# Kernel optimization log

Measured on AMD Instinct MI355X. Metric: run time of the kernel, lower is better.

The kernel has to match this reference:

```python
import jax, jax.numpy as jnp
import numpy as np


def setup_inputs() -> dict:
    key = jax.random.key(0)
    k1, k2, k3, k4 = jax.random.split(key, 4)
    bs, n, f_in, f_out, n_head = 4, 2048, 64, 64, 8
    h = jax.random.normal(k1, (bs, n, f_in), dtype=jnp.float32)
    adj = jnp.ones((bs, n, n), dtype=bool)  # accepted by forward but unused
    # xavier-uniform-like init scales
    w = jax.random.uniform(k2, (n_head, f_in, f_out), dtype=jnp.float32,
                           minval=-1.0, maxval=1.0) * np.sqrt(6.0 / (f_in + f_out))
    a_src = jax.random.uniform(k3, (n_head, f_out, 1), dtype=jnp.float32,
                               minval=-1.0, maxval=1.0) * np.sqrt(6.0 / (f_out + 1))
    a_dst = jax.random.uniform(k4, (n_head, f_out, 1), dtype=jnp.float32,
                               minval=-1.0, maxval=1.0) * np.sqrt(6.0 / (f_out + 1))
    bias_p = jnp.zeros((f_out,), dtype=jnp.float32)
    return {"h": h, "adj": adj, "w": w, "a_src": a_src, "a_dst": a_dst, "bias_p": bias_p}


def reference(h, adj, w, a_src, a_dst, bias_p):
    # h: [b, n, f_in], w: [h, f_in, f_out]
    h_prime = jnp.einsum('bnf,hfo->bhno', h, w)          # [b, h, n, f_out]
    t = jnp.tanh(h_prime)
    attn_src = jnp.einsum('bhno,ho->bhn', t, a_src[..., 0])  # [b, h, n]
    attn_dst = jnp.einsum('bhno,ho->bhn', t, a_dst[..., 0])  # [b, h, n]
    # attn[b,h,i,j] = src[b,h,i] + dst[b,h,j]  (dense; adj unused in original)
    attn = attn_src[..., :, None] + attn_dst[..., None, :]   # [b, h, n, n]
    attn = jnp.where(attn >= 0, attn, 0.2 * attn)            # leaky_relu(0.2)
    attn = jax.nn.softmax(attn, axis=-1)
    # dropout p=0.0 -> identity
    out = jnp.einsum('bhij,bhjo->bhio', attn, h_prime)       # [b, h, n, f_out]
    return out + bias_p
```

## Files before the change

kernel.cpp:

```cpp
#include <hip/hip_runtime.h>
#include <hip/hip_bf16.h>

#define NN 2048
#define FF 64
#define NH 8
#define BDIM 4
#define BH 32

typedef __attribute__((ext_vector_type(8))) short short8;
typedef __attribute__((ext_vector_type(4))) float floatx4;
typedef __attribute__((ext_vector_type(4))) unsigned uint4v;

__device__ __forceinline__ float LDIN(const void* p, size_t i, int b16) {
    return b16 ? __bfloat162float(((const __hip_bfloat16*)p)[i]) : ((const float*)p)[i];
}
__device__ __forceinline__ unsigned packhi(float f0, float f1) {
    return __builtin_amdgcn_perm(__float_as_uint(f1), __float_as_uint(f0), 0x07060302);
}
__device__ __forceinline__ float hitrunc(float x) {
    return __uint_as_float(__float_as_uint(x) & 0xFFFF0000u);
}
__device__ __forceinline__ ushort bf16bits(float v) {
    __hip_bfloat16 b = __float2bfloat16(v);
    return __builtin_bit_cast(ushort, b);
}
__device__ __forceinline__ int SWZ(int row, int col) {
    return row * 64 + ((((col >> 3) ^ (row & 7)) << 3) | (col & 7));
}
__device__ __forceinline__ float fast_tanh(float v) {
    float ex = __expf(2.0f * v);
    return 1.0f - 2.0f * __builtin_amdgcn_rcpf(ex + 1.0f);
}
__device__ __forceinline__ int sniff_b16(const void* h) {
    unsigned word = ((const unsigned*)h)[threadIdx.x & 63];
    unsigned lowexp = (word >> 7) & 0xFFu;
    bool plaus = (lowexp >= 96u && lowexp <= 159u);
    unsigned long long m = __ballot(plaus);
    return (__popcll(m) >= 48) ? 1 : 0;
}

__global__ __launch_bounds__(256) void k_prep(
    const void* __restrict__ h, const void* __restrict__ w,
    ushort* __restrict__ wF, int* __restrict__ flagOut)
{
    const int hd = blockIdx.x, t = threadIdx.x;
    __shared__ int sb16;
    if (t < 64) {
        int f = sniff_b16(h);
        if (t == 0) { sb16 = f; if (hd == 0) flagOut[0] = f; }
    }
    __syncthreads();
    const int b16 = sb16;

#pragma unroll
    for (int g = 0; g < 2; ++g) {
        int gi = t * 2 + g;
        int ml = gi & 15, q = (gi >> 4) & 3, kc = (gi >> 6) & 1, nt = (gi >> 7) & 3;
        int n = nt * 16 + ml, kb = kc * 32 + q * 8;
        size_t off = (size_t)hd * 4096 + ((nt * 2 + kc) * 4 + q) * 128 + ml * 8;
        if (b16) {
            const ushort* wp = (const ushort*)w + (size_t)hd * FF * FF;
            ushort hi[8];
#pragma unroll
            for (int j = 0; j < 8; ++j) hi[j] = wp[(kb + j) * FF + n];
            *(uint4v*)&wF[off] = __builtin_bit_cast(uint4v, *(short8*)hi);
            short8 z = {0, 0, 0, 0, 0, 0, 0, 0};
            *(uint4v*)&wF[off + 32768] = __builtin_bit_cast(uint4v, z);
        } else {
            const float* wp = (const float*)w + (size_t)hd * FF * FF;
            float x[8];
#pragma unroll
            for (int j = 0; j < 8; ++j) x[j] = wp[(kb + j) * FF + n];
            uint4v hv = { packhi(x[0], x[1]), packhi(x[2], x[3]),
                          packhi(x[4], x[5]), packhi(x[6], x[7]) };
            uint4v lv = { packhi(x[0] - hitrunc(x[0]), x[1] - hitrunc(x[1])),
                          packhi(x[2] - hitrunc(x[2]), x[3] - hitrunc(x[3])),
                          packhi(x[4] - hitrunc(x[4]), x[5] - hitrunc(x[5])),
                          packhi(x[6] - hitrunc(x[6]), x[7] - hitrunc(x[7])) };
            *(uint4v*)&wF[off] = hv;
            *(uint4v*)&wF[off + 32768] = lv;
        }
    }
}

__global__ __launch_bounds__(256) void k_proj(
    const void* __restrict__ h, const ushort* __restrict__ wF,
    const void* __restrict__ asrc, const void* __restrict__ adst,
    ushort* __restrict__ hpTt, float* __restrict__ rArr,
    float* __restrict__ edHa, float* __restrict__ edLa)
{
    const int t  = threadIdx.x;
    const int rt = blockIdx.x & 31;
    const int hd = (blockIdx.x >> 5) & 7;
    const int b  = blockIdx.x >> 8;
    const int bh = b * NH + hd;
    const int r0 = rt * 64;

    __shared__ int sb16;
    __shared__ ushort aHi[64 * 64];
    __shared__ ushort aLo[64 * 64];
    __shared__ ushort trans[64 * 64];
    if (t < 64) {
        int f = sniff_b16(h);
        if (t == 0) sb16 = f;
    }
    __syncthreads();
    const int b16 = sb16;

    const int lane = t & 63, wv = t >> 6;
    const int ml = lane & 15, q = lane >> 4;

    if (b16) {
        const ushort* hsrc = (const ushort*)h + (size_t)(b * NN + r0) * FF;
#pragma unroll
        for (int g0 = 0; g0 < 2; ++g0) {
            int g = t + g0 * 256;
            int row = g >> 3, c8 = (g & 7) * 8;
            uint4v u = *(const uint4v*)(hsrc + row * FF + c8);
            *(uint4v*)&aHi[SWZ(row, c8)] = u;
        }
    } else {
        const float* hsrc = (const float*)h + (size_t)(b * NN + r0) * FF;
#pragma unroll
        for (int g0 = 0; g0 < 4; ++g0) {
            int g = t + g0 * 256;
            int row = g >> 4, c4 = (g & 15) * 4;
            floatx4 x = *(const floatx4*)(hsrc + row * FF + c4);
            uint2 hi2 = { packhi(x[0], x[1]), packhi(x[2], x[3]) };
            uint2 lo2 = { packhi(x[0] - hitrunc(x[0]), x[1] - hitrunc(x[1])),
                          packhi(x[2] - hitrunc(x[2]), x[3] - hitrunc(x[3])) };
            *(uint2*)&aHi[SWZ(row, c4)] = hi2;
            *(uint2*)&aLo[SWZ(row, c4)] = lo2;
        }
    }
    __syncthreads();

    short8 ah[2], al[2];
#pragma unroll
    for (int kc = 0; kc < 2; ++kc) {
        ah[kc] = *(const short8*)&aHi[SWZ(wv * 16 + ml, kc * 32 + q * 8)];
        if (!b16) al[kc] = *(const short8*)&aLo[SWZ(wv * 16 + ml, kc * 32 + q * 8)];
    }
    short8 bhf[4][2], blf[4][2];
    const ushort* wfh = wF + (size_t)hd * 4096;
#pragma unroll
    for (int nt = 0; nt < 4; ++nt)
#pragma unroll
        for (int kc = 0; kc < 2; ++kc) {
            size_t off = ((nt * 2 + kc) * 4 + q) * 128 + ml * 8;
            bhf[nt][kc] = __builtin_bit_cast(short8, *(const uint4v*)&wfh[off]);
            if (!b16) blf[nt][kc] = __builtin_bit_cast(short8, *(const uint4v*)&wfh[off + 32768]);
        }

    float aS[4], aD[4];
#pragma unroll
    for (int nt = 0; nt < 4; ++nt) {
        aS[nt] = LDIN(asrc, hd * FF + nt * 16 + ml, b16);
        aD[nt] = LDIN(adst, hd * FF + nt * 16 + ml, b16);
    }

    floatx4 acc[4];
#pragma unroll
    for (int nt = 0; nt < 4; ++nt) {
        floatx4 a = {0.f, 0.f, 0.f, 0.f};
        if (b16) {
#pragma unroll
            for (int kc = 0; kc < 2; ++kc)
                a = __builtin_amdgcn_mfma_f32_16x16x32_bf16(ah[kc], bhf[nt][kc], a, 0, 0, 0);
        } else {
#pragma unroll
            for (int kc = 0; kc < 2; ++kc) {
                a = __builtin_amdgcn_mfma_f32_16x16x32_bf16(ah[kc], bhf[nt][kc], a, 0, 0, 0);
                a = __builtin_amdgcn_mfma_f32_16x16x32_bf16(ah[kc], blf[nt][kc], a, 0, 0, 0);
                a = __builtin_amdgcn_mfma_f32_16x16x32_bf16(al[kc], bhf[nt][kc], a, 0, 0, 0);
            }
        }
        acc[nt] = a;
    }

#pragma unroll
    for (int nt = 0; nt < 4; ++nt) {
        ushort b0 = bf16bits(acc[nt][0]), b1 = bf16bits(acc[nt][1]);
        ushort b2 = bf16bits(acc[nt][2]), b3 = bf16bits(acc[nt][3]);
        uint2 pk = { (unsigned)b0 | ((unsigned)b1 << 16),
                     (unsigned)b2 | ((unsigned)b3 << 16) };
        *(uint2*)&trans[SWZ(nt * 16 + ml, wv * 16 + q * 4)] = pk;
    }

    float ps[4] = {0.f, 0.f, 0.f, 0.f}, pd[4] = {0.f, 0.f, 0.f, 0.f};
#pragma unroll
    for (int nt = 0; nt < 4; ++nt)
#pragma unroll
        for (int reg = 0; reg < 4; ++reg) {
            float tv = fast_tanh(acc[nt][reg]);
            ps[reg] += tv * aS[nt];
            pd[reg] += tv * aD[nt];
        }
#pragma unroll
    for (int msk = 1; msk < 16; msk <<= 1)
#pragma unroll
        for (int reg = 0; reg < 4; ++reg) {
            ps[reg] += __shfl_xor(ps[reg], msk, 64);
            pd[reg] += __shfl_xor(pd[reg], msk, 64);
        }
    if (ml == 0) {
#pragma unroll
        for (int reg = 0; reg < 4; ++reg) {
            int i = bh * NN + r0 + wv * 16 + q * 4 + reg;
            float sv = ps[reg], dv = pd[reg];
            rArr[i] = __expf(-0.8f * sv);
            edHa[i] = __expf(dv);
            edLa[i] = __expf(0.2f * dv);
        }
    }
    __syncthreads();
    {
        const int o = t >> 2, part = (t & 3) * 16;
        uint4v v0 = *(const uint4v*)&trans[SWZ(o, part)];
        uint4v v1 = *(const uint4v*)&trans[SWZ(o, part + 8)];
        ushort* dst = hpTt + (((size_t)bh * 32 + rt) * 64 + o) * 64 + part;
        *(uint4v*)dst = v0;
        *(uint4v*)(dst + 8) = v1;
    }
}

__global__ __launch_bounds__(512) void k_attn(
    const ushort* __restrict__ hpTt, const float* __restrict__ rArr,
    const float* __restrict__ edHa, const float* __restrict__ edLa,
    const void* __restrict__ bias, const int* __restrict__ flag,
    void* __restrict__ out)
{
    const int b16 = flag[0];
    const int t = threadIdx.x;
    const int wv = t >> 6, lane = t & 63;
    const int ml = lane & 15, q = lane >> 4;
    const int bh = blockIdx.x & 31;
    const int i0 = (blockIdx.x >> 5) * 128 + wv * 16;

    __shared__ ushort Bc[4][64 * 64];
    __shared__ __align__(16) float ehS[NN];
    __shared__ __align__(16) float elS[NN];

    ((floatx4*)ehS)[t] = ((const floatx4*)(edHa + bh * NN))[t];
    ((floatx4*)elS)[t] = ((const floatx4*)(edLa + bh * NN))[t];

    const ushort* src = hpTt + (size_t)bh * NN * FF;
    const float r = rArr[bh * NN + i0 + ml];

    const short8 ONESB = {0x3F80, 0x3F80, 0x3F80, 0x3F80,
                          0x3F80, 0x3F80, 0x3F80, 0x3F80};

    floatx4 acc[4];
#pragma unroll
    for (int nt = 0; nt < 4; ++nt) acc[nt] = (floatx4){0.f, 0.f, 0.f, 0.f};
    floatx4 accD = {0.f, 0.f, 0.f, 0.f};

    auto stage = [&](int c) {
        uint4v u = *(const uint4v*)(src + (size_t)c * 4096 + t * 8);
        *(uint4v*)&Bc[c & 3][SWZ(t >> 3, (t & 7) * 8)] = u;
    };

    auto compute = [&](int c) {
        const int j0 = c * 64, buf = c & 3;
#pragma unroll
        for (int ks = 0; ks < 2; ++ks) {
            const int col = ks * 32 + q * 8;
            floatx4 eh0 = *(const floatx4*)&ehS[j0 + col];
            floatx4 eh1 = *(const floatx4*)&ehS[j0 + col + 4];
            floatx4 el0 = *(const floatx4*)&elS[j0 + col];
            floatx4 el1 = *(const floatx4*)&elS[j0 + col + 4];
            short8 Bf[4];
#pragma unroll
            for (int nt = 0; nt < 4; ++nt)
                Bf[nt] = *(const short8*)&Bc[buf][SWZ(nt * 16 + ml, col)];
            float p[8];
#pragma unroll
            for (int j = 0; j < 4; ++j) {
                p[j]     = fmaxf(eh0[j], r * el0[j]);
                p[j + 4] = fmaxf(eh1[j], r * el1[j]);
            }
            uint4v hv = { packhi(p[0], p[1]), packhi(p[2], p[3]),
                          packhi(p[4], p[5]), packhi(p[6], p[7]) };
            short8 PH = __builtin_bit_cast(short8, hv);
#pragma unroll
            for (int nt = 0; nt < 4; ++nt)
                acc[nt] = __builtin_amdgcn_mfma_f32_16x16x32_bf16(PH, Bf[nt], acc[nt], 0, 0, 0);
            accD = __builtin_amdgcn_mfma_f32_16x16x32_bf16(PH, ONESB, accD, 0, 0, 0);
        }
    };

    stage(0); stage(1);
    __syncthreads();
    for (int c = 0; c < 32; c += 2) {
        if (c + 2 < 32) { stage(c + 2); stage(c + 3); }
        compute(c);
        compute(c + 1);
        __syncthreads();
    }

    float biasv[4];
#pragma unroll
    for (int nt = 0; nt < 4; ++nt) biasv[nt] = LDIN(bias, nt * 16 + ml, b16);

#pragma unroll
    for (int reg = 0; reg < 4; ++reg) {
        float inv = 1.0f / accD[reg];
        int i = i0 + q * 4 + reg;
#pragma unroll
        for (int nt = 0; nt < 4; ++nt) {
            float val = acc[nt][reg] * inv + biasv[nt];
            size_t oi = ((size_t)bh * NN + i) * FF + nt * 16 + ml;
            if (b16) ((__hip_bfloat16*)out)[oi] = __float2bfloat16(val);
            else     ((float*)out)[oi] = val;
        }
    }
}

extern "C" void kernel_launch(void* const* d_in, const int* in_sizes, int n_in,
                              void* d_out, int out_size, void* d_ws, size_t ws_size,
                              hipStream_t stream) {
    const void* h    = d_in[0];
    const void* w    = d_in[2];
    const void* asrc = d_in[3];
    const void* adst = d_in[4];
    const void* bias = d_in[5];

    float* ws = (float*)d_ws;
    int*    flag = (int*)ws;
    ushort* hpTt = (ushort*)(ws + 16);
    float*  rArr = (float*)(hpTt + (size_t)BH * NN * FF);
    float*  edHa = rArr + BH * NN;
    float*  edLa = edHa + BH * NN;
    ushort* wF   = (ushort*)(edLa + BH * NN);

    k_prep<<<NH, 256, 0, stream>>>(h, w, wF, flag);
    k_proj<<<BDIM * NH * 32, 256, 0, stream>>>(h, wF, asrc, adst,
                                               hpTt, rArr, edHa, edLa);
    k_attn<<<BH * 16, 512, 0, stream>>>(hpTt, rArr, edHa, edLa,
                                        bias, flag, d_out);
}
```

Before: 138.7 us.

## Fuse prep, projection and attention into one cooperative kernel with grid sync

Replaces the three-kernel pipeline with one cooperative kernel of 256 blocks. Each block builds its own W fragments in shared memory, projects four row tiles, writes the intermediates, then passes a grid-wide sync before running attention over 256 query rows per block with two row groups sharing each staged B tile. This removes two kernel launches and the separate weight-prep pass, and doubles reuse of each staged chunk. In exchange it relies on cooperative launch co-residency and grid sync, uses 64 KB shared memory per block, and the attention phase runs on only 256 blocks with double buffering, where before it had 512 blocks. The fallback k_attn also drops from four shared buffers to two.

```diff
diff --git a/kernel.cpp b/kernel.cpp
--- a/kernel.cpp
+++ b/kernel.cpp
@@ -1,4 +1,5 @@
 #include <hip/hip_runtime.h>
+#include <hip/hip_cooperative_groups.h>
 #include <hip/hip_bf16.h>
 
 #define NN 2048
@@ -6,6 +7,8 @@
 #define NH 8
 #define BDIM 4
 #define BH 32
+
+namespace cg = cooperative_groups;
 
 typedef __attribute__((ext_vector_type(8))) short short8;
 typedef __attribute__((ext_vector_type(4))) float floatx4;
@@ -37,6 +40,283 @@
     bool plaus = (lowexp >= 96u && lowexp <= 159u);
     unsigned long long m = __ballot(plaus);
     return (__popcll(m) >= 48) ? 1 : 0;
+}
+
+__global__ __launch_bounds__(512, 2) void k_fused(
+    const void* __restrict__ h, const void* __restrict__ w,
+    const void* __restrict__ asrc, const void* __restrict__ adst,
+    const void* __restrict__ bias, void* __restrict__ out,
+    ushort* __restrict__ hpTt, float* __restrict__ rArr,
+    float* __restrict__ edHa, float* __restrict__ edLa)
+{
+    __shared__ __align__(16) ushort SH[32768];
+    __shared__ int sb16;
+
+    const int t = threadIdx.x;
+    const int bid = blockIdx.x;
+    const int lane = t & 63, wv = t >> 6;
+    const int ml = lane & 15, q = lane >> 4;
+
+    if (t < 64) {
+        int f = sniff_b16(h);
+        if (t == 0) sb16 = f;
+    }
+    __syncthreads();
+    const int b16 = sb16;
+
+    const int gt0 = bid * 4;
+    const int hd = (gt0 >> 5) & 7;
+    const int b  = gt0 >> 8;
+    const int bh = b * NH + hd;
+
+    {
+        const int n = t & 63, kq = (t >> 6) * 4;
+        if (b16) {
+            const ushort* wp = (const ushort*)w + (size_t)hd * FF * FF;
+#pragma unroll
+            for (int g = 0; g < 2; ++g) {
+                int kb = g * 32 + kq;
+                ushort v0 = wp[(kb + 0) * FF + n];
+                ushort v1 = wp[(kb + 1) * FF + n];
+                ushort v2 = wp[(kb + 2) * FF + n];
+                ushort v3 = wp[(kb + 3) * FF + n];
+                uint2 pk = { (unsigned)v0 | ((unsigned)v1 << 16),
+                             (unsigned)v2 | ((unsigned)v3 << 16) };
+                *(uint2*)&SH[SWZ(n, kb)] = pk;
+            }
+        } else {
+            const float* wp = (const float*)w + (size_t)hd * FF * FF;
+#pragma unroll
+            for (int g = 0; g < 2; ++g) {
+                int kb = g * 32 + kq;
+                float x0 = wp[(kb + 0) * FF + n];
+                float x1 = wp[(kb + 1) * FF + n];
+                float x2 = wp[(kb + 2) * FF + n];
+                float x3 = wp[(kb + 3) * FF + n];
+                uint2 hi2 = { packhi(x0, x1), packhi(x2, x3) };
+                uint2 lo2 = { packhi(x0 - hitrunc(x0), x1 - hitrunc(x1)),
+                              packhi(x2 - hitrunc(x2), x3 - hitrunc(x3)) };
+                *(uint2*)&SH[SWZ(n, kb)] = hi2;
+                *(uint2*)&SH[4096 + SWZ(n, kb)] = lo2;
+            }
+        }
+    }
+    __syncthreads();
+
+    short8 bhf[4][2], blf[4][2];
+#pragma unroll
+    for (int nt = 0; nt < 4; ++nt)
+#pragma unroll
+        for (int kc = 0; kc < 2; ++kc) {
+            bhf[nt][kc] = *(const short8*)&SH[SWZ(nt * 16 + ml, kc * 32 + q * 8)];
+            if (!b16) blf[nt][kc] = *(const short8*)&SH[4096 + SWZ(nt * 16 + ml, kc * 32 + q * 8)];
+        }
+    float aS[4], aD[4];
+#pragma unroll
+    for (int nt = 0; nt < 4; ++nt) {
+        aS[nt] = LDIN(asrc, hd * FF + nt * 16 + ml, b16);
+        aD[nt] = LDIN(adst, hd * FF + nt * 16 + ml, b16);
+    }
+
+    const int tp = wv >> 2, wl = wv & 3;
+    for (int it2 = 0; it2 < 2; ++it2) {
+        {
+            const int ts = t >> 8, local = t & 255;
+            const int rt = (gt0 + it2 * 2 + ts) & 31;
+            if (b16) {
+                const ushort* hsrc = (const ushort*)h + (size_t)(b * NN + rt * 64) * FF;
+#pragma unroll
+                for (int g0 = 0; g0 < 2; ++g0) {
+                    int g = local + g0 * 256;
+                    int row = g >> 3, c8 = (g & 7) * 8;
+                    uint4v u = *(const uint4v*)(hsrc + row * FF + c8);
+                    *(uint4v*)&SH[8192 + ts * 4096 + SWZ(row, c8)] = u;
+                }
+            } else {
+                const float* hsrc = (const float*)h + (size_t)(b * NN + rt * 64) * FF;
+#pragma unroll
+                for (int g0 = 0; g0 < 4; ++g0) {
+                    int g = local + g0 * 256;
+                    int row = g >> 4, c4 = (g & 15) * 4;
+                    floatx4 x = *(const floatx4*)(hsrc + row * FF + c4);
+                    uint2 hi2 = { packhi(x[0], x[1]), packhi(x[2], x[3]) };
+                    uint2 lo2 = { packhi(x[0] - hitrunc(x[0]), x[1] - hitrunc(x[1])),
+                                  packhi(x[2] - hitrunc(x[2]), x[3] - hitrunc(x[3])) };
+                    *(uint2*)&SH[8192 + ts * 4096 + SWZ(row, c4)] = hi2;
+                    *(uint2*)&SH[16384 + ts * 4096 + SWZ(row, c4)] = lo2;
+                }
+            }
+        }
+        __syncthreads();
+
+        short8 ah[2], al[2];
+#pragma unroll
+        for (int kc = 0; kc < 2; ++kc) {
+            ah[kc] = *(const short8*)&SH[8192 + tp * 4096 + SWZ(wl * 16 + ml, kc * 32 + q * 8)];
+            if (!b16) al[kc] = *(const short8*)&SH[16384 + tp * 4096 + SWZ(wl * 16 + ml, kc * 32 + q * 8)];
+        }
+        floatx4 acc[4];
+#pragma unroll
+        for (int nt = 0; nt < 4; ++nt) {
+            floatx4 a = {0.f, 0.f, 0.f, 0.f};
+            if (b16) {
+#pragma unroll
+                for (int kc = 0; kc < 2; ++kc)
+                    a = __builtin_amdgcn_mfma_f32_16x16x32_bf16(ah[kc], bhf[nt][kc], a, 0, 0, 0);
+            } else {
+#pragma unroll
+                for (int kc = 0; kc < 2; ++kc) {
+                    a = __builtin_amdgcn_mfma_f32_16x16x32_bf16(ah[kc], bhf[nt][kc], a, 0, 0, 0);
+                    a = __builtin_amdgcn_mfma_f32_16x16x32_bf16(ah[kc], blf[nt][kc], a, 0, 0, 0);
+                    a = __builtin_amdgcn_mfma_f32_16x16x32_bf16(al[kc], bhf[nt][kc], a, 0, 0, 0);
+                }
+            }
+            acc[nt] = a;
+        }
+#pragma unroll
+        for (int nt = 0; nt < 4; ++nt) {
+            ushort b0 = bf16bits(acc[nt][0]), b1 = bf16bits(acc[nt][1]);
+            ushort b2 = bf16bits(acc[nt][2]), b3 = bf16bits(acc[nt][3]);
+            uint2 pk = { (unsigned)b0 | ((unsigned)b1 << 16),
+                         (unsigned)b2 | ((unsigned)b3 << 16) };
+            *(uint2*)&SH[24576 + tp * 4096 + SWZ(nt * 16 + ml, wl * 16 + q * 4)] = pk;
+        }
+        float ps[4] = {0.f, 0.f, 0.f, 0.f}, pd[4] = {0.f, 0.f, 0.f, 0.f};
+#pragma unroll
+        for (int nt = 0; nt < 4; ++nt)
+#pragma unroll
+            for (int reg = 0; reg < 4; ++reg) {
+                float tv = fast_tanh(acc[nt][reg]);
+                ps[reg] += tv * aS[nt];
+                pd[reg] += tv * aD[nt];
+            }
+#pragma unroll
+        for (int msk = 1; msk < 16; msk <<= 1)
+#pragma unroll
+            for (int reg = 0; reg < 4; ++reg) {
+                ps[reg] += __shfl_xor(ps[reg], msk, 64);
+                pd[reg] += __shfl_xor(pd[reg], msk, 64);
+            }
+        if (ml == 0) {
+            const int rt = (gt0 + it2 * 2 + tp) & 31;
+#pragma unroll
+            for (int reg = 0; reg < 4; ++reg) {
+                int i = bh * NN + rt * 64 + wl * 16 + q * 4 + reg;
+                float sv = ps[reg], dv = pd[reg];
+                rArr[i] = __expf(-0.8f * sv);
+                edHa[i] = __expf(dv);
+                edLa[i] = __expf(0.2f * dv);
+            }
+        }
+        __syncthreads();
+        {
+            const int ts = t >> 8, local = t & 255;
+            const int rt = (gt0 + it2 * 2 + ts) & 31;
+            const int o = local >> 2, part = (local & 3) * 16;
+            uint4v v0 = *(const uint4v*)&SH[24576 + ts * 4096 + SWZ(o, part)];
+            uint4v v1 = *(const uint4v*)&SH[24576 + ts * 4096 + SWZ(o, part + 8)];
+            ushort* dst = hpTt + (((size_t)bh * 32 + rt) * 64 + o) * 64 + part;
+            *(uint4v*)dst = v0;
+            *(uint4v*)(dst + 8) = v1;
+        }
+        __syncthreads();
+    }
+
+    __threadfence();
+    cg::this_grid().sync();
+    __threadfence();
+
+    const int bh2 = bid >> 3;
+    const int seg = bid & 7;
+    const ushort* src = hpTt + (size_t)bh2 * NN * FF;
+
+    ((floatx4*)(SH + 8192))[t]  = ((const floatx4*)(edHa + bh2 * NN))[t];
+    ((floatx4*)(SH + 16384))[t] = ((const floatx4*)(edLa + bh2 * NN))[t];
+
+    float r2[2];
+#pragma unroll
+    for (int g2 = 0; g2 < 2; ++g2)
+        r2[g2] = rArr[bh2 * NN + seg * 256 + g2 * 128 + wv * 16 + ml];
+
+    const short8 ONESB = {0x3F80, 0x3F80, 0x3F80, 0x3F80,
+                          0x3F80, 0x3F80, 0x3F80, 0x3F80};
+
+    floatx4 acc2[2][4];
+#pragma unroll
+    for (int g2 = 0; g2 < 2; ++g2)
+#pragma unroll
+        for (int nt = 0; nt < 4; ++nt) acc2[g2][nt] = (floatx4){0.f, 0.f, 0.f, 0.f};
+    floatx4 accD0 = {0.f, 0.f, 0.f, 0.f};
+    floatx4 accD1 = {0.f, 0.f, 0.f, 0.f};
+
+    auto stage = [&](int c) {
+        uint4v u = *(const uint4v*)(src + (size_t)c * 4096 + t * 8);
+        *(uint4v*)&SH[(c & 1) * 4096 + SWZ(t >> 3, (t & 7) * 8)] = u;
+    };
+    auto compute = [&](int c) {
+        const int j0 = c * 64, bufo = (c & 1) * 4096;
+        const float* ehS = (const float*)(SH + 8192);
+        const float* elS = (const float*)(SH + 16384);
+#pragma unroll
+        for (int ks = 0; ks < 2; ++ks) {
+            const int col = ks * 32 + q * 8;
+            floatx4 eh0 = *(const floatx4*)&ehS[j0 + col];
+            floatx4 eh1 = *(const floatx4*)&ehS[j0 + col + 4];
+            floatx4 el0 = *(const floatx4*)&elS[j0 + col];
+            floatx4 el1 = *(const floatx4*)&elS[j0 + col + 4];
+            short8 Bf[4];
+#pragma unroll
+            for (int nt = 0; nt < 4; ++nt)
+                Bf[nt] = *(const short8*)&SH[bufo + SWZ(nt * 16 + ml, col)];
+#pragma unroll
+            for (int g2 = 0; g2 < 2; ++g2) {
+                float p[8];
+#pragma unroll
+                for (int j = 0; j < 4; ++j) {
+                    p[j]     = fmaxf(eh0[j], r2[g2] * el0[j]);
+                    p[j + 4] = fmaxf(eh1[j], r2[g2] * el1[j]);
+                }
+                uint4v hv = { packhi(p[0], p[1]), packhi(p[2], p[3]),
+                              packhi(p[4], p[5]), packhi(p[6], p[7]) };
+                short8 PH = __builtin_bit_cast(short8, hv);
+#pragma unroll
+                for (int nt = 0; nt < 4; ++nt)
+                    acc2[g2][nt] = __builtin_amdgcn_mfma_f32_16x16x32_bf16(PH, Bf[nt], acc2[g2][nt], 0, 0, 0);
+                if (g2 == 0) accD0 = __builtin_amdgcn_mfma_f32_16x16x32_bf16(PH, ONESB, accD0, 0, 0, 0);
+                else         accD1 = __builtin_amdgcn_mfma_f32_16x16x32_bf16(PH, ONESB, accD1, 0, 0, 0);
+            }
+        }
+    };
+
+    stage(0);
+    __syncthreads();
+    for (int c = 0; c < 32; ++c) {
+        if (c + 1 < 32) stage(c + 1);
+        compute(c);
+        __syncthreads();
+    }
+
+    float biasv[4];
+#pragma unroll
+    for (int nt = 0; nt < 4; ++nt) biasv[nt] = LDIN(bias, nt * 16 + ml, b16);
+
+#pragma unroll
+    for (int g2 = 0; g2 < 2; ++g2) {
+        const int i0 = seg * 256 + g2 * 128 + wv * 16;
+#pragma unroll
+        for (int reg = 0; reg < 4; ++reg) {
+            float dv = g2 ? accD1[reg] : accD0[reg];
+            float inv = 1.0f / dv;
+            int i = i0 + q * 4 + reg;
+#pragma unroll
+            for (int nt = 0; nt < 4; ++nt) {
+                float val = acc2[g2][nt][reg] * inv + biasv[nt];
+                size_t oi = ((size_t)bh2 * NN + i) * FF + nt * 16 + ml;
+                if (b16) ((__hip_bfloat16*)out)[oi] = __float2bfloat16(val);
+                else     ((float*)out)[oi] = val;
+            }
+        }
+    }
 }
 
 __global__ __launch_bounds__(256) void k_prep(
@@ -51,7 +331,6 @@
     }
     __syncthreads();
     const int b16 = sb16;
-
 #pragma unroll
     for (int g = 0; g < 2; ++g) {
         int gi = t * 2 + g;
@@ -106,7 +385,6 @@
     }
     __syncthreads();
     const int b16 = sb16;
-
     const int lane = t & 63, wv = t >> 6;
     const int ml = lane & 15, q = lane >> 4;
 
@@ -151,14 +429,12 @@
             bhf[nt][kc] = __builtin_bit_cast(short8, *(const uint4v*)&wfh[off]);
             if (!b16) blf[nt][kc] = __builtin_bit_cast(short8, *(const uint4v*)&wfh[off + 32768]);
         }
-
     float aS[4], aD[4];
 #pragma unroll
     for (int nt = 0; nt < 4; ++nt) {
         aS[nt] = LDIN(asrc, hd * FF + nt * 16 + ml, b16);
         aD[nt] = LDIN(adst, hd * FF + nt * 16 + ml, b16);
     }
-
     floatx4 acc[4];
 #pragma unroll
     for (int nt = 0; nt < 4; ++nt) {
@@ -177,7 +453,6 @@
         }
         acc[nt] = a;
     }
-
 #pragma unroll
     for (int nt = 0; nt < 4; ++nt) {
         ushort b0 = bf16bits(acc[nt][0]), b1 = bf16bits(acc[nt][1]);
@@ -186,7 +461,6 @@
                      (unsigned)b2 | ((unsigned)b3 << 16) };
         *(uint2*)&trans[SWZ(nt * 16 + ml, wv * 16 + q * 4)] = pk;
     }
-
     float ps[4] = {0.f, 0.f, 0.f, 0.f}, pd[4] = {0.f, 0.f, 0.f, 0.f};
 #pragma unroll
     for (int nt = 0; nt < 4; ++nt)
@@ -237,7 +511,8 @@
     const int bh = blockIdx.x & 31;
     const int i0 = (blockIdx.x >> 5) * 128 + wv * 16;
 
-    __shared__ ushort Bc[4][64 * 64];
+    __shared__ ushort Bc0[64 * 64];
+    __shared__ ushort Bc1[64 * 64];
     __shared__ __align__(16) float ehS[NN];
     __shared__ __align__(16) float elS[NN];
 
@@ -246,10 +521,8 @@
 
     const ushort* src = hpTt + (size_t)bh * NN * FF;
     const float r = rArr[bh * NN + i0 + ml];
-
     const short8 ONESB = {0x3F80, 0x3F80, 0x3F80, 0x3F80,
                           0x3F80, 0x3F80, 0x3F80, 0x3F80};
-
     floatx4 acc[4];
 #pragma unroll
     for (int nt = 0; nt < 4; ++nt) acc[nt] = (floatx4){0.f, 0.f, 0.f, 0.f};
@@ -257,11 +530,12 @@
 
     auto stage = [&](int c) {
         uint4v u = *(const uint4v*)(src + (size_t)c * 4096 + t * 8);
-        *(uint4v*)&Bc[c & 3][SWZ(t >> 3, (t & 7) * 8)] = u;
+        ushort* d = (c & 1) ? Bc1 : Bc0;
+        *(uint4v*)&d[SWZ(t >> 3, (t & 7) * 8)] = u;
     };
-
     auto compute = [&](int c) {
-        const int j0 = c * 64, buf = c & 3;
+        const int j0 = c * 64;
+        const ushort* buf = (c & 1) ? Bc1 : Bc0;
 #pragma unroll
         for (int ks = 0; ks < 2; ++ks) {
             const int col = ks * 32 + q * 8;
@@ -272,7 +546,7 @@
             short8 Bf[4];
 #pragma unroll
             for (int nt = 0; nt < 4; ++nt)
-                Bf[nt] = *(const short8*)&Bc[buf][SWZ(nt * 16 + ml, col)];
+                Bf[nt] = *(const short8*)&buf[SWZ(nt * 16 + ml, col)];
             float p[8];
 #pragma unroll
             for (int j = 0; j < 4; ++j) {
@@ -289,19 +563,17 @@
         }
     };
 
-    stage(0); stage(1);
-    __syncthreads();
-    for (int c = 0; c < 32; c += 2) {
-        if (c + 2 < 32) { stage(c + 2); stage(c + 3); }
+    stage(0);
+    __syncthreads();
+    for (int c = 0; c < 32; ++c) {
+        if (c + 1 < 32) stage(c + 1);
         compute(c);
-        compute(c + 1);
         __syncthreads();
     }
 
     float biasv[4];
 #pragma unroll
     for (int nt = 0; nt < 4; ++nt) biasv[nt] = LDIN(bias, nt * 16 + ml, b16);
-
 #pragma unroll
     for (int reg = 0; reg < 4; ++reg) {
         float inv = 1.0f / accD[reg];
@@ -324,6 +596,7 @@
     const void* asrc = d_in[3];
     const void* adst = d_in[4];
     const void* bias = d_in[5];
+    void* out = d_out;
 
     float* ws = (float*)d_ws;
     int*    flag = (int*)ws;
@@ -333,9 +606,17 @@
     float*  edLa = edHa + BH * NN;
     ushort* wF   = (ushort*)(edLa + BH * NN);
 
-    k_prep<<<NH, 256, 0, stream>>>(h, w, wF, flag);
-    k_proj<<<BDIM * NH * 32, 256, 0, stream>>>(h, wF, asrc, adst,
-                                               hpTt, rArr, edHa, edLa);
-    k_attn<<<BH * 16, 512, 0, stream>>>(hpTt, rArr, edHa, edLa,
-                                        bias, flag, d_out);
-}
+    void* args[] = { (void*)&h, (void*)&w, (void*)&asrc, (void*)&adst,
+                     (void*)&bias, (void*)&out,
+                     (void*)&hpTt, (void*)&rArr, (void*)&edHa, (void*)&edLa };
+    hipError_t err = hipLaunchCooperativeKernel(
+        reinterpret_cast<void*>(k_fused), dim3(256), dim3(512), args, 0, stream);
+    if (err != hipSuccess) {
+        (void)hipGetLastError();
+        k_prep<<<NH, 256, 0, stream>>>(h, w, wF, flag);
+        k_proj<<<BDIM * NH * 32, 256, 0, stream>>>(h, wF, asrc, adst,
+                                                   hpTt, rArr, edHa, edLa);
+        k_attn<<<BH * 16, 512, 0, stream>>>(hpTt, rArr, edHa, edLa,
+                                            bias, flag, d_out);
+    }
+}
```

After: 253.7 us. 82.9% more time.
